# Kernel tuning notes

Hardware: AMD Instinct MI355X
Metric: run time of the kernel (lower is better)

## Reference

```python
import jax, jax.numpy as jnp
import numpy as np

N_CAM, N_PTS, N_OBS = 2000, 500000, 5000000


def setup_inputs() -> dict:
    key = jax.random.key(0)
    k1, k2, k3, k4, k5, k6 = jax.random.split(key, 6)
    # SE3 poses: [tx, ty, tz, qx, qy, qz, qw] (pypose layout), unit quaternions
    t = jax.random.normal(k1, (N_CAM, 3), dtype=jnp.float32) * 5.0
    t = t.at[:, 2].set(jax.random.uniform(k2, (N_CAM,), minval=100.0, maxval=200.0))
    q = jax.random.normal(k3, (N_CAM, 4), dtype=jnp.float32)
    q = q / jnp.linalg.norm(q, axis=-1, keepdims=True)
    poses = jnp.concatenate([t, q], axis=-1)  # [N_CAM, 7]
    points = jax.random.normal(k4, (N_PTS, 3), dtype=jnp.float32) * 5.0  # [N_PTS, 3]
    # Pinhole intrinsics
    K = jnp.array([[1000.0, 0.0, 640.0], [0.0, 1000.0, 360.0], [0.0, 0.0, 1.0]], dtype=jnp.float32)
    observes = jax.random.normal(k5, (N_OBS, 2), dtype=jnp.float32) * 100.0 + 500.0
    ki, kj = jax.random.split(k6)
    cidx = jax.random.randint(ki, (N_OBS,), 0, N_CAM, dtype=jnp.int64)
    pidx = jax.random.randint(kj, (N_OBS,), 0, N_PTS, dtype=jnp.int64)
    return {"observes": observes, "K": K, "poses": poses, "points": points, "cidx": cidx, "pidx": pidx}


def _se3_act(pose7, pts):
    # pose7: [N,7] (t, q) with q=(x,y,z,w); pts: [N,3]
    t = pose7[:, :3]
    qv = pose7[:, 3:6]
    qw = pose7[:, 6:7]
    # p' = p + 2 * qv x (qv x p + w p) + t   (unit-quaternion rotation)
    uv = jnp.cross(qv, pts)
    return pts + 2.0 * jnp.cross(qv, uv + qw * pts) + t


def reference(observes, K, poses, points, cidx, pidx):
    p_cam = _se3_act(poses[cidx], points[pidx])  # [N_OBS, 3] camera-frame points
    img = p_cam @ K.T                            # [N_OBS, 3] homogeneous pixels
    projs = img[:, :2] / img[:, 2:3]             # [N_OBS, 2]
    return (projs - observes).reshape(-1)        # [N_OBS * 2]
```

## Files before the change

kernel.cpp:

```cpp
#include <hip/hip_runtime.h>


typedef float vfloat4 __attribute__((ext_vector_type(4)));
typedef int   vint4   __attribute__((ext_vector_type(4)));

__global__ __launch_bounds__(256) void resid_kernel4(
    const float* __restrict__ obs,
    const float* __restrict__ Kmat,
    const float* __restrict__ poses,
    const float* __restrict__ points,
    const int*   __restrict__ cidx,
    const int*   __restrict__ pidx,
    float*       __restrict__ out,
    int n)
{
    int t = blockIdx.x * blockDim.x + threadIdx.x;
    int base = t * 4;

    float fx = Kmat[0], cx = Kmat[2];
    float fy = Kmat[4], cy = Kmat[5];

    if (base + 4 <= n) {
        vint4   c4  = __builtin_nontemporal_load((const vint4*)(cidx + base));
        vint4   p4  = __builtin_nontemporal_load((const vint4*)(pidx + base));
        vfloat4 o01 = __builtin_nontemporal_load((const vfloat4*)(obs + 2 * base));
        vfloat4 o23 = __builtin_nontemporal_load((const vfloat4*)(obs + 2 * base + 4));

        int cc[4] = {c4.x, c4.y, c4.z, c4.w};
        int pp[4] = {p4.x, p4.y, p4.z, p4.w};

        float P[4][3];
        #pragma unroll
        for (int k = 0; k < 4; ++k) {
            const float* pt = points + 3 * pp[k];
            P[k][0] = pt[0]; P[k][1] = pt[1]; P[k][2] = pt[2];
        }
        float Q[4][7];
        #pragma unroll
        for (int k = 0; k < 4; ++k) {
            const float* ps = poses + 7 * cc[k];
            #pragma unroll
            for (int j = 0; j < 7; ++j) Q[k][j] = ps[j];
        }

        float res[8];
        #pragma unroll
        for (int k = 0; k < 4; ++k) {
            float px = P[k][0], py = P[k][1], pz = P[k][2];
            float tx = Q[k][0], ty = Q[k][1], tz = Q[k][2];
            float qx = Q[k][3], qy = Q[k][4], qz = Q[k][5], qw = Q[k][6];

            float ux = qy * pz - qz * py;
            float uy = qz * px - qx * pz;
            float uz = qx * py - qy * px;
            float wx = ux + qw * px;
            float wy = uy + qw * py;
            float wz = uz + qw * pz;
            float ccx = qy * wz - qz * wy;
            float ccy = qz * wx - qx * wz;
            float ccz = qx * wy - qy * wx;
            float X = px + 2.0f * ccx + tx;
            float Y = py + 2.0f * ccy + ty;
            float Z = pz + 2.0f * ccz + tz;

            float invz = 1.0f / Z;
            res[2 * k]     = fx * X * invz + cx;
            res[2 * k + 1] = fy * Y * invz + cy;
        }

        vfloat4 r0 = {res[0] - o01.x, res[1] - o01.y, res[2] - o01.z, res[3] - o01.w};
        vfloat4 r1 = {res[4] - o23.x, res[5] - o23.y, res[6] - o23.z, res[7] - o23.w};
        __builtin_nontemporal_store(r0, (vfloat4*)(out + 2 * base));
        __builtin_nontemporal_store(r1, (vfloat4*)(out + 2 * base + 4));
    } else {
        for (int i = base; i < n; ++i) {
            int c = cidx[i];
            int p = pidx[i];
            const float* ps = poses + 7 * c;
            const float* pt = points + 3 * p;
            float px = pt[0], py = pt[1], pz = pt[2];
            float tx = ps[0], ty = ps[1], tz = ps[2];
            float qx = ps[3], qy = ps[4], qz = ps[5], qw = ps[6];

            float ux = qy * pz - qz * py;
            float uy = qz * px - qx * pz;
            float uz = qx * py - qy * px;
            float wx = ux + qw * px;
            float wy = uy + qw * py;
            float wz = uz + qw * pz;
            float ccx = qy * wz - qz * wy;
            float ccy = qz * wx - qx * wz;
            float ccz = qx * wy - qy * wx;
            float X = px + 2.0f * ccx + tx;
            float Y = py + 2.0f * ccy + ty;
            float Z = pz + 2.0f * ccz + tz;

            float invz = 1.0f / Z;
            out[2 * i]     = fx * X * invz + cx - obs[2 * i];
            out[2 * i + 1] = fy * Y * invz + cy - obs[2 * i + 1];
        }
    }
}

extern "C" void kernel_launch(void* const* d_in, const int* in_sizes, int n_in,
                              void* d_out, int out_size, void* d_ws, size_t ws_size,
                              hipStream_t stream) {
    const float* obs    = (const float*)d_in[0];
    const float* Kmat   = (const float*)d_in[1];
    const float* poses  = (const float*)d_in[2];
    const float* points = (const float*)d_in[3];
    const int*   cidx   = (const int*)d_in[4];
    const int*   pidx   = (const int*)d_in[5];
    float*       out    = (float*)d_out;

    int n = in_sizes[4];
    int block = 256;
    int per_block = block * 4;
    int grid = (n + per_block - 1) / per_block;
    resid_kernel4<<<grid, block, 0, stream>>>(obs, Kmat, poses, points, cidx, pidx, out, n);
}
```

Measured before the change: 189.2 us.

## Repack points and poses into 16-byte padded layout for vector gathers

Adds two pre-pass kernels that copy points into float4 slots and poses into pairs of float4 in workspace memory. The main kernel then gathers each point with one 16-byte load and each pose with two, instead of several scalar loads at unaligned strides. The cost is two extra launches plus a re-read and re-write of the point array (about 6 MB read, 8 MB written) on every call. A scalar fallback kernel runs when the workspace is too small.

```diff
diff --git a/kernel.cpp b/kernel.cpp
--- a/kernel.cpp
+++ b/kernel.cpp
@@ -4,14 +4,36 @@
 typedef float vfloat4 __attribute__((ext_vector_type(4)));
 typedef int   vint4   __attribute__((ext_vector_type(4)));
 
-__global__ __launch_bounds__(256) void resid_kernel4(
-    const float* __restrict__ obs,
-    const float* __restrict__ Kmat,
-    const float* __restrict__ poses,
-    const float* __restrict__ points,
-    const int*   __restrict__ cidx,
-    const int*   __restrict__ pidx,
-    float*       __restrict__ out,
+__global__ __launch_bounds__(256) void pad_points(
+    const float* __restrict__ src, vfloat4* __restrict__ dst, int n_pts)
+{
+    int i = blockIdx.x * blockDim.x + threadIdx.x;
+    if (i >= n_pts) return;
+    const float* s = src + 3 * i;
+    vfloat4 v = {s[0], s[1], s[2], 0.0f};
+    dst[i] = v;
+}
+
+__global__ __launch_bounds__(256) void pad_poses(
+    const float* __restrict__ src, vfloat4* __restrict__ dst, int n_cam)
+{
+    int i = blockIdx.x * blockDim.x + threadIdx.x;
+    if (i >= n_cam) return;
+    const float* s = src + 7 * i;
+    vfloat4 a = {s[0], s[1], s[2], s[3]};
+    vfloat4 b = {s[4], s[5], s[6], 0.0f};
+    dst[2 * i]     = a;
+    dst[2 * i + 1] = b;
+}
+
+__global__ __launch_bounds__(256) void resid_kernel4p(
+    const float*   __restrict__ obs,
+    const float*   __restrict__ Kmat,
+    const vfloat4* __restrict__ poses_pad,
+    const vfloat4* __restrict__ points_pad,
+    const int*     __restrict__ cidx,
+    const int*     __restrict__ pidx,
+    float*         __restrict__ out,
     int n)
 {
     int t = blockIdx.x * blockDim.x + threadIdx.x;
@@ -29,26 +51,21 @@
         int cc[4] = {c4.x, c4.y, c4.z, c4.w};
         int pp[4] = {p4.x, p4.y, p4.z, p4.w};
 
-        float P[4][3];
+        vfloat4 P[4], QA[4], QB[4];
+        #pragma unroll
+        for (int k = 0; k < 4; ++k) P[k] = points_pad[pp[k]];
         #pragma unroll
         for (int k = 0; k < 4; ++k) {
-            const float* pt = points + 3 * pp[k];
-            P[k][0] = pt[0]; P[k][1] = pt[1]; P[k][2] = pt[2];
-        }
-        float Q[4][7];
-        #pragma unroll
-        for (int k = 0; k < 4; ++k) {
-            const float* ps = poses + 7 * cc[k];
-            #pragma unroll
-            for (int j = 0; j < 7; ++j) Q[k][j] = ps[j];
+            QA[k] = poses_pad[2 * cc[k]];
+            QB[k] = poses_pad[2 * cc[k] + 1];
         }
 
         float res[8];
         #pragma unroll
         for (int k = 0; k < 4; ++k) {
-            float px = P[k][0], py = P[k][1], pz = P[k][2];
-            float tx = Q[k][0], ty = Q[k][1], tz = Q[k][2];
-            float qx = Q[k][3], qy = Q[k][4], qz = Q[k][5], qw = Q[k][6];
+            float px = P[k].x, py = P[k].y, pz = P[k].z;
+            float tx = QA[k].x, ty = QA[k].y, tz = QA[k].z;
+            float qx = QA[k].w, qy = QB[k].x, qz = QB[k].y, qw = QB[k].z;
 
             float ux = qy * pz - qz * py;
             float uy = qz * px - qx * pz;
@@ -74,13 +91,12 @@
         __builtin_nontemporal_store(r1, (vfloat4*)(out + 2 * base + 4));
     } else {
         for (int i = base; i < n; ++i) {
-            int c = cidx[i];
-            int p = pidx[i];
-            const float* ps = poses + 7 * c;
-            const float* pt = points + 3 * p;
-            float px = pt[0], py = pt[1], pz = pt[2];
-            float tx = ps[0], ty = ps[1], tz = ps[2];
-            float qx = ps[3], qy = ps[4], qz = ps[5], qw = ps[6];
+            vfloat4 P  = points_pad[pidx[i]];
+            vfloat4 QA = poses_pad[2 * cidx[i]];
+            vfloat4 QB = poses_pad[2 * cidx[i] + 1];
+            float px = P.x, py = P.y, pz = P.z;
+            float tx = QA.x, ty = QA.y, tz = QA.z;
+            float qx = QA.w, qy = QB.x, qz = QB.y, qw = QB.z;
 
             float ux = qy * pz - qz * py;
             float uy = qz * px - qx * pz;
@@ -102,6 +118,36 @@
     }
 }
 
+__global__ __launch_bounds__(256) void resid_fallback(
+    const float* __restrict__ obs, const float* __restrict__ Kmat,
+    const float* __restrict__ poses, const float* __restrict__ points,
+    const int* __restrict__ cidx, const int* __restrict__ pidx,
+    float* __restrict__ out, int n)
+{
+    int i = blockIdx.x * blockDim.x + threadIdx.x;
+    if (i >= n) return;
+    const float* ps = poses + 7 * cidx[i];
+    const float* pt = points + 3 * pidx[i];
+    float px = pt[0], py = pt[1], pz = pt[2];
+    float tx = ps[0], ty = ps[1], tz = ps[2];
+    float qx = ps[3], qy = ps[4], qz = ps[5], qw = ps[6];
+    float ux = qy * pz - qz * py;
+    float uy = qz * px - qx * pz;
+    float uz = qx * py - qy * px;
+    float wx = ux + qw * px;
+    float wy = uy + qw * py;
+    float wz = uz + qw * pz;
+    float ccx = qy * wz - qz * wy;
+    float ccy = qz * wx - qx * wz;
+    float ccz = qx * wy - qy * wx;
+    float X = px + 2.0f * ccx + tx;
+    float Y = py + 2.0f * ccy + ty;
+    float Z = pz + 2.0f * ccz + tz;
+    float invz = 1.0f / Z;
+    out[2 * i]     = Kmat[0] * X * invz + Kmat[2] - obs[2 * i];
+    out[2 * i + 1] = Kmat[4] * Y * invz + Kmat[5] - obs[2 * i + 1];
+}
+
 extern "C" void kernel_launch(void* const* d_in, const int* in_sizes, int n_in,
                               void* d_out, int out_size, void* d_ws, size_t ws_size,
                               hipStream_t stream) {
@@ -113,9 +159,27 @@
     const int*   pidx   = (const int*)d_in[5];
     float*       out    = (float*)d_out;
 
-    int n = in_sizes[4];
-    int block = 256;
-    int per_block = block * 4;
+    int n     = in_sizes[4];
+    int n_cam = in_sizes[2] / 7;
+    int n_pts = in_sizes[3] / 3;
+
+    size_t pts_bytes  = (size_t)n_pts * 16;
+    size_t pose_bytes = (size_t)n_cam * 32;
+
+    if (ws_size < pts_bytes + pose_bytes) {
+        resid_fallback<<<(n + 255) / 256, 256, 0, stream>>>(
+            obs, Kmat, poses, points, cidx, pidx, out, n);
+        return;
+    }
+
+    vfloat4* points_pad = (vfloat4*)d_ws;
+    vfloat4* poses_pad  = (vfloat4*)((char*)d_ws + pts_bytes);
+
+    pad_points<<<(n_pts + 255) / 256, 256, 0, stream>>>(points, points_pad, n_pts);
+    pad_poses<<<(n_cam + 255) / 256, 256, 0, stream>>>(poses, poses_pad, n_cam);
+
+    int per_block = 256 * 4;
     int grid = (n + per_block - 1) / per_block;
-    resid_kernel4<<<grid, block, 0, stream>>>(obs, Kmat, poses, points, cidx, pidx, out, n);
+    resid_kernel4p<<<grid, 256, 0, stream>>>(
+        obs, Kmat, poses_pad, points_pad, cidx, pidx, out, n);
 }
```

After: 188.5 us. About the same (-0.4%).
